# Performance work log

Hardware: AMD Instinct MI355X
Metric: run time of the kernel (lower is better)

## Reference

```python
import jax, jax.numpy as jnp
import numpy as np

BINS = 256
H = 2048
N = 2_000_000


def _tensor2image(x):
    # standard GAN denorm: [-1,1] -> [0,1]
    return (x + 1.0) * 0.5


def _cdf(vals):
    # torch.histc(bins=256, min=0, max=256): unit-width bins, values in [0,255]
    idx = jnp.clip(jnp.floor(vals), 0, BINS - 1).astype(jnp.int32)
    hist = jnp.zeros((BINS,), jnp.float32).at[idx].add(1.0)
    return jnp.cumsum(hist) / hist.sum()


def _trans_table(ref_cdf, adj_cdf):
    # cal_trans: for i in 1..255, first j in 1..255 with adj[j-1] <= ref[i] <= adj[j]
    i_vals = ref_cdf[1:]  # [255]
    cond = (adj_cdf[:-1][None, :] <= i_vals[:, None]) & (i_vals[:, None] <= adj_cdf[1:][None, :])  # [255,255]
    found = cond.any(axis=1)
    first_j = jnp.argmax(cond, axis=1) + 1
    tab = jnp.where(found, first_j, jnp.arange(1, BINS))  # unmatched entries keep identity
    tab = jnp.concatenate([jnp.zeros((1,), tab.dtype), tab])
    tab = tab.at[BINS - 1].set(BINS - 1)
    return tab.astype(jnp.float32)


def _hist_match(dst_img, ref_img, i0, i1, i2, i3):
    # dst_img, ref_img: [3,H,W]; indices: [N]
    dst_align = dst_img[:, i0, i1]  # [3,N]
    ref_align = ref_img[:, i2, i3]  # [3,N]
    cdf_dst = jax.vmap(_cdf)(dst_align)  # [3,256]
    cdf_ref = jax.vmap(_cdf)(ref_align)  # [3,256]
    tables = jax.vmap(_trans_table)(cdf_dst, cdf_ref)  # [3,256]
    bins = jnp.clip(dst_align, 0, BINS - 1).astype(jnp.int32)  # int() truncation on [0,255]
    new_align = jnp.take_along_axis(tables, bins, axis=1)  # [3,N]
    return dst_img.at[:, i0, i1].set(new_align)


def reference(input_data, target_data, mask_src, mask_tar, index0, index1, index2, index3, ref_data):
    inp = _tensor2image(input_data) * 255.0
    tgt = _tensor2image(target_data) * 255.0
    ref = _tensor2image(ref_data) * 255.0
    h = mask_src.shape[2]
    m_src = jnp.broadcast_to(mask_src, (1, 3, h, h))
    m_tar = jnp.broadcast_to(mask_tar, (1, 3, h, h))
    input_masked = inp * m_src
    target_masked = (tgt * m_tar)[0]  # [3,H,W]
    ref_masked = (ref * m_src)[0]     # [3,H,W]
    i0, i1, i2, i3 = index0[0], index1[0], index2[0], index3[0]
    matched = _hist_match(ref_masked, target_masked, i0, i1, i2, i3)[None]  # [1,3,H,W]
    input_match = jax.lax.stop_gradient(matched) * m_src  # no_grad in original
    return jnp.mean((input_masked - input_match) ** 2)


def setup_inputs() -> dict:
    key = jax.random.key(0)
    ks = jax.random.split(key, 9)
    inp = {
        "input_data": jax.random.uniform(ks[0], (1, 3, H, H), jnp.float32, -1.0, 1.0),
        "target_data": jax.random.uniform(ks[1], (1, 3, H, H), jnp.float32, -1.0, 1.0),
        "mask_src": (jax.random.uniform(ks[2], (1, 1, H, H)) > 0.5).astype(jnp.float32),
        "mask_tar": (jax.random.uniform(ks[3], (1, 1, H, H)) > 0.5).astype(jnp.float32),
        "index0": jax.random.randint(ks[4], (1, N), 0, H, jnp.int32),
        "index1": jax.random.randint(ks[5], (1, N), 0, H, jnp.int32),
        "index2": jax.random.randint(ks[6], (1, N), 0, H, jnp.int32),
        "index3": jax.random.randint(ks[7], (1, N), 0, H, jnp.int32),
        "ref_data": jax.random.uniform(ks[8], (1, 3, H, H), jnp.float32, -1.0, 1.0),
    }
    return inp
```

## Files before the change

### kernel.cpp

```cpp
#include <hip/hip_runtime.h>

#define HDIM 2048
#define HH (HDIM * HDIM)
#define NIDX 2000000
#define BINS 256
#define NCOPY 16
#define TL_BLOCKS 2048
#define WH_BLOCKS 2048
#define NWIN 8

#define PART_OFF     0
#define TAB_OFF      16384
#define HIST_OFF     20480
#define PACKED_D_OFF 1048576
#define PACKED_R_OFF 17825792

__global__ __launch_bounds__(256) void pack_kernel(
    const float* __restrict__ ref, const float* __restrict__ tgt,
    const float* __restrict__ msrc, const float* __restrict__ mtar,
    unsigned* __restrict__ packed_d, unsigned* __restrict__ packed_r,
    unsigned* __restrict__ hist)
{
    const int gtid = blockIdx.x * 256 + threadIdx.x;
    const int stride = gridDim.x * 256;

    for (int k = gtid; k < NCOPY * 6 * BINS; k += stride) hist[k] = 0;

    for (int g = gtid; g < HH / 4; g += stride) {
        const int p = g * 4;
        const float4 ms4 = *(const float4*)(msrc + p);
        const float4 mt4 = *(const float4*)(mtar + p);
        const float ms[4] = {ms4.x, ms4.y, ms4.z, ms4.w};
        const float mt[4] = {mt4.x, mt4.y, mt4.z, mt4.w};
        unsigned od[4] = {0, 0, 0, 0}, orr[4] = {0, 0, 0, 0};
#pragma unroll
        for (int c = 0; c < 3; c++) {
            const float4 rv = *(const float4*)(ref + c * HH + p);
            const float4 tv = *(const float4*)(tgt + c * HH + p);
            const float r[4] = {rv.x, rv.y, rv.z, rv.w};
            const float tt[4] = {tv.x, tv.y, tv.z, tv.w};
#pragma unroll
            for (int k = 0; k < 4; k++) {
                const float vd = ((r[k] + 1.0f) * 0.5f) * 255.0f * ms[k];
                const float vr = ((tt[k] + 1.0f) * 0.5f) * 255.0f * mt[k];
                const unsigned bd = (unsigned)(int)fminf(fmaxf(floorf(vd), 0.0f), 255.0f);
                const unsigned br = (unsigned)(int)fminf(fmaxf(floorf(vr), 0.0f), 255.0f);
                od[k]  |= bd << (8 * c);
                orr[k] |= br << (8 * c);
            }
        }
        *(uint4*)(packed_d + p) = make_uint4(od[0], od[1], od[2], od[3]);
        *(uint4*)(packed_r + p) = make_uint4(orr[0], orr[1], orr[2], orr[3]);
    }
}

__global__ __launch_bounds__(256) void whist_kernel(
    unsigned* __restrict__ packed_d, const unsigned* __restrict__ packed_r,
    const int* __restrict__ i0, const int* __restrict__ i1,
    const int* __restrict__ i2, const int* __restrict__ i3,
    unsigned* __restrict__ hist)
{
    __shared__ unsigned lhist[6 * BINS];
    for (int k = threadIdx.x; k < 6 * BINS; k += 256) lhist[k] = 0;
    __syncthreads();

    unsigned z0 = 0, z1 = 0, z2 = 0, z3 = 0, z4 = 0, z5 = 0;
    unsigned char* sampled = (unsigned char*)packed_d;
    const int stride = gridDim.x * 256;

    for (int w = 0; w < NWIN; w++) {
        for (int q = blockIdx.x * 256 + threadIdx.x; q < NIDX / 4; q += stride) {
            const int4 a = ((const int4*)i0)[q];
            const int4 b = ((const int4*)i1)[q];
            const int pd[4] = {a.x * HDIM + b.x, a.y * HDIM + b.y,
                               a.z * HDIM + b.z, a.w * HDIM + b.w};
#pragma unroll
            for (int k = 0; k < 4; k++) {
                if ((pd[k] >> 19) == w) {
                    const unsigned wd = packed_d[pd[k]];
                    sampled[pd[k] * 4 + 3] = 1;
                    const unsigned d0 =  wd        & 255u;
                    const unsigned d1 = (wd >> 8 ) & 255u;
                    const unsigned d2 = (wd >> 16) & 255u;
                    if (d0) atomicAdd(&lhist[           d0], 1u); else z0++;
                    if (d1) atomicAdd(&lhist[1 * BINS + d1], 1u); else z1++;
                    if (d2) atomicAdd(&lhist[2 * BINS + d2], 1u); else z2++;
                }
            }
        }
    }
    for (int w = 0; w < NWIN; w++) {
        for (int q = blockIdx.x * 256 + threadIdx.x; q < NIDX / 4; q += stride) {
            const int4 c = ((const int4*)i2)[q];
            const int4 d = ((const int4*)i3)[q];
            const int pr[4] = {c.x * HDIM + d.x, c.y * HDIM + d.y,
                               c.z * HDIM + d.z, c.w * HDIM + d.w};
#pragma unroll
            for (int k = 0; k < 4; k++) {
                if ((pr[k] >> 19) == w) {
                    const unsigned wr = packed_r[pr[k]];
                    const unsigned r0 =  wr        & 255u;
                    const unsigned r1 = (wr >> 8 ) & 255u;
                    const unsigned r2 = (wr >> 16) & 255u;
                    if (r0) atomicAdd(&lhist[3 * BINS + r0], 1u); else z3++;
                    if (r1) atomicAdd(&lhist[4 * BINS + r1], 1u); else z4++;
                    if (r2) atomicAdd(&lhist[5 * BINS + r2], 1u); else z5++;
                }
            }
        }
    }

    if (z0) atomicAdd(&lhist[0 * BINS], z0);
    if (z1) atomicAdd(&lhist[1 * BINS], z1);
    if (z2) atomicAdd(&lhist[2 * BINS], z2);
    if (z3) atomicAdd(&lhist[3 * BINS], z3);
    if (z4) atomicAdd(&lhist[4 * BINS], z4);
    if (z5) atomicAdd(&lhist[5 * BINS], z5);
    __syncthreads();
    unsigned* h = hist + (blockIdx.x & (NCOPY - 1)) * (6 * BINS);
    for (int k = threadIdx.x; k < 6 * BINS; k += 256) {
        const unsigned v = lhist[k];
        if (v) atomicAdd(&h[k], v);
    }
}

__global__ __launch_bounds__(256) void table_kernel(
    const unsigned* __restrict__ hist, float* __restrict__ tabg)
{
    __shared__ float    cdf[6 * BINS];
    __shared__ unsigned wsum[4];

    const int t    = threadIdx.x;
    const int lane = t & 63;
    const int wid  = t >> 6;

    for (int ch = 0; ch < 6; ch++) {
        unsigned x = 0;
#pragma unroll
        for (int cp = 0; cp < NCOPY; cp++) x += hist[cp * (6 * BINS) + ch * BINS + t];
#pragma unroll
        for (int d = 1; d < 64; d <<= 1) {
            const unsigned y = __shfl_up(x, d, 64);
            if (lane >= d) x += y;
        }
        if (lane == 63) wsum[wid] = x;
        __syncthreads();
        unsigned prefix = 0;
        for (int w = 0; w < wid; w++) prefix += wsum[w];
        x += prefix;
        cdf[ch * BINS + t] = (float)x / 2000000.0f;
        __syncthreads();
    }
    for (int c = 0; c < 3; c++) {
        float o;
        if (t == 0)             o = 0.0f;
        else if (t == BINS - 1) o = 255.0f;
        else {
            const float v = cdf[c * BINS + t];
            const float* arr = cdf + (3 + c) * BINS;
            int lo = 0, hi = 256;
            while (lo < hi) { const int mid = (lo + hi) >> 1; if (arr[mid] < v) lo = mid + 1; else hi = mid; }
            const int J0 = ((lo > 1) ? lo : 1) - 1;
            int lo2 = 0, hi2 = 256;
            while (lo2 < hi2) { const int mid = (lo2 + hi2) >> 1; if (arr[mid] <= v) lo2 = mid + 1; else hi2 = mid; }
            const int J1 = ((lo2 - 1) < 254 ? (lo2 - 1) : 254);
            const bool found = (lo2 >= 1) && (J0 <= J1);
            o = found ? (float)(J0 + 1) : (float)t;
        }
        tabg[c * BINS + t] = o;
    }
}

__global__ __launch_bounds__(256) void tabloss_kernel(
    const float* __restrict__ inp, const float* __restrict__ ref,
    const float* __restrict__ msrc, const float* __restrict__ tabg,
    const unsigned* __restrict__ packed_d, double* __restrict__ partials)
{
    __shared__ float  tab[3 * BINS];
    __shared__ double red[256];

    const int t = threadIdx.x;
    for (int k = t; k < 3 * BINS; k += 256) tab[k] = tabg[k];
    __syncthreads();

    double local = 0.0;
    const int stride = gridDim.x * 256;
    for (int g = blockIdx.x * 256 + t; g < HH / 4; g += stride) {
        const int p = g * 4;
        const float4 mv = *(const float4*)(msrc + p);
        const uint4 pw = *(const uint4*)(packed_d + p);
        const unsigned samp[4] = {pw.x >> 24, pw.y >> 24, pw.z >> 24, pw.w >> 24};
        const float m[4] = {mv.x, mv.y, mv.z, mv.w};
#pragma unroll
        for (int c = 0; c < 3; c++) {
            const float4 rv = *(const float4*)(ref + c * HH + p);
            const float4 iv = *(const float4*)(inp + c * HH + p);
            const float r[4] = {rv.x, rv.y, rv.z, rv.w};
            const float x4[4] = {iv.x, iv.y, iv.z, iv.w};
            float s = 0.0f;
#pragma unroll
            for (int k = 0; k < 4; k++) {
                const float mm = m[k];
                const float refm = ((r[k] + 1.0f) * 0.5f) * 255.0f * mm;
                const float inpm = ((x4[k] + 1.0f) * 0.5f) * 255.0f * mm;
                float matchv;
                if (samp[k]) {
                    const int bidx = (int)fminf(fmaxf(refm, 0.0f), 255.0f);
                    matchv = tab[c * BINS + bidx];
                } else {
                    matchv = refm;
                }
                const float dd = inpm - matchv * mm;
                s += dd * dd;
            }
            local += (double)s;
        }
    }
    red[t] = local;
    __syncthreads();
    for (int s2 = 128; s2 > 0; s2 >>= 1) {
        if (t < s2) red[t] += red[t + s2];
        __syncthreads();
    }
    if (t == 0) partials[blockIdx.x] = red[0];
}

__global__ __launch_bounds__(256) void finalize_kernel(
    const double* __restrict__ partials, float* __restrict__ out)
{
    const int t = threadIdx.x;
    double s = 0.0;
    for (int k = t; k < TL_BLOCKS; k += 256) s += partials[k];
    __shared__ double red[256];
    red[t] = s;
    __syncthreads();
    for (int s2 = 128; s2 > 0; s2 >>= 1) {
        if (t < s2) red[t] += red[t + s2];
        __syncthreads();
    }
    if (t == 0) out[0] = (float)(red[0] / (double)(3 * HH));
}

extern "C" void kernel_launch(void* const* d_in, const int* in_sizes, int n_in,
                              void* d_out, int out_size, void* d_ws, size_t ws_size,
                              hipStream_t stream)
{
    const float* input_data  = (const float*)d_in[0];
    const float* target_data = (const float*)d_in[1];
    const float* mask_src    = (const float*)d_in[2];
    const float* mask_tar    = (const float*)d_in[3];
    const int*   i0          = (const int*)d_in[4];
    const int*   i1          = (const int*)d_in[5];
    const int*   i2          = (const int*)d_in[6];
    const int*   i3          = (const int*)d_in[7];
    const float* ref_data    = (const float*)d_in[8];
    float* out = (float*)d_out;

    char* ws = (char*)d_ws;
    double*   partials = (double*)(ws + PART_OFF);
    float*    tabg     = (float*)(ws + TAB_OFF);
    unsigned* hist     = (unsigned*)(ws + HIST_OFF);
    unsigned* packed_d = (unsigned*)(ws + PACKED_D_OFF);
    unsigned* packed_r = (unsigned*)(ws + PACKED_R_OFF);

    pack_kernel<<<2048, 256, 0, stream>>>(ref_data, target_data, mask_src, mask_tar,
                                          packed_d, packed_r, hist);
    whist_kernel<<<WH_BLOCKS, 256, 0, stream>>>(packed_d, packed_r, i0, i1, i2, i3, hist);
    table_kernel<<<1, 256, 0, stream>>>(hist, tabg);
    tabloss_kernel<<<TL_BLOCKS, 256, 0, stream>>>(input_data, ref_data, mask_src, tabg,
                                                  packed_d, partials);
    finalize_kernel<<<1, 256, 0, stream>>>(partials, out);
}
```

Before: 371.7 us.

## Precompute flat gather indices and move sampled flags to a separate byte array

```diff
diff --git a/kernel.cpp b/kernel.cpp
--- a/kernel.cpp
+++ b/kernel.cpp
@@ -12,19 +12,37 @@
 #define PART_OFF     0
 #define TAB_OFF      16384
 #define HIST_OFF     20480
-#define PACKED_D_OFF 1048576
-#define PACKED_R_OFF 17825792
+#define FLAGS_OFF    131072
+#define PD_OFF       4325376
+#define PR_OFF       12713984
+#define PACKED_D_OFF 21102592
+#define PACKED_R_OFF 37879808
 
 __global__ __launch_bounds__(256) void pack_kernel(
     const float* __restrict__ ref, const float* __restrict__ tgt,
     const float* __restrict__ msrc, const float* __restrict__ mtar,
+    const int* __restrict__ i0, const int* __restrict__ i1,
+    const int* __restrict__ i2, const int* __restrict__ i3,
     unsigned* __restrict__ packed_d, unsigned* __restrict__ packed_r,
-    unsigned* __restrict__ hist)
+    int* __restrict__ pdArr, int* __restrict__ prArr,
+    unsigned* __restrict__ hist, unsigned* __restrict__ flags32)
 {
     const int gtid = blockIdx.x * 256 + threadIdx.x;
     const int stride = gridDim.x * 256;
 
     for (int k = gtid; k < NCOPY * 6 * BINS; k += stride) hist[k] = 0;
+    for (int k = gtid; k < HH / 4; k += stride) flags32[k] = 0;
+
+    for (int s = gtid; s < NIDX / 4; s += stride) {
+        const int4 a = ((const int4*)i0)[s];
+        const int4 b = ((const int4*)i1)[s];
+        const int4 c = ((const int4*)i2)[s];
+        const int4 d = ((const int4*)i3)[s];
+        ((int4*)pdArr)[s] = make_int4(a.x * HDIM + b.x, a.y * HDIM + b.y,
+                                      a.z * HDIM + b.z, a.w * HDIM + b.w);
+        ((int4*)prArr)[s] = make_int4(c.x * HDIM + d.x, c.y * HDIM + d.y,
+                                      c.z * HDIM + d.z, c.w * HDIM + d.w);
+    }
 
     for (int g = gtid; g < HH / 4; g += stride) {
         const int p = g * 4;
@@ -55,30 +73,26 @@
 }
 
 __global__ __launch_bounds__(256) void whist_kernel(
-    unsigned* __restrict__ packed_d, const unsigned* __restrict__ packed_r,
-    const int* __restrict__ i0, const int* __restrict__ i1,
-    const int* __restrict__ i2, const int* __restrict__ i3,
-    unsigned* __restrict__ hist)
+    const unsigned* __restrict__ packed_d, const unsigned* __restrict__ packed_r,
+    const int* __restrict__ pdArr, const int* __restrict__ prArr,
+    unsigned char* __restrict__ flags, unsigned* __restrict__ hist)
 {
     __shared__ unsigned lhist[6 * BINS];
     for (int k = threadIdx.x; k < 6 * BINS; k += 256) lhist[k] = 0;
     __syncthreads();
 
     unsigned z0 = 0, z1 = 0, z2 = 0, z3 = 0, z4 = 0, z5 = 0;
-    unsigned char* sampled = (unsigned char*)packed_d;
     const int stride = gridDim.x * 256;
 
     for (int w = 0; w < NWIN; w++) {
         for (int q = blockIdx.x * 256 + threadIdx.x; q < NIDX / 4; q += stride) {
-            const int4 a = ((const int4*)i0)[q];
-            const int4 b = ((const int4*)i1)[q];
-            const int pd[4] = {a.x * HDIM + b.x, a.y * HDIM + b.y,
-                               a.z * HDIM + b.z, a.w * HDIM + b.w};
+            const int4 pv = ((const int4*)pdArr)[q];
+            const int pd[4] = {pv.x, pv.y, pv.z, pv.w};
 #pragma unroll
             for (int k = 0; k < 4; k++) {
                 if ((pd[k] >> 19) == w) {
                     const unsigned wd = packed_d[pd[k]];
-                    sampled[pd[k] * 4 + 3] = 1;
+                    flags[pd[k]] = 1;
                     const unsigned d0 =  wd        & 255u;
                     const unsigned d1 = (wd >> 8 ) & 255u;
                     const unsigned d2 = (wd >> 16) & 255u;
@@ -91,10 +105,8 @@
     }
     for (int w = 0; w < NWIN; w++) {
         for (int q = blockIdx.x * 256 + threadIdx.x; q < NIDX / 4; q += stride) {
-            const int4 c = ((const int4*)i2)[q];
-            const int4 d = ((const int4*)i3)[q];
-            const int pr[4] = {c.x * HDIM + d.x, c.y * HDIM + d.y,
-                               c.z * HDIM + d.z, c.w * HDIM + d.w};
+            const int4 pv = ((const int4*)prArr)[q];
+            const int pr[4] = {pv.x, pv.y, pv.z, pv.w};
 #pragma unroll
             for (int k = 0; k < 4; k++) {
                 if ((pr[k] >> 19) == w) {
@@ -174,7 +186,7 @@
 __global__ __launch_bounds__(256) void tabloss_kernel(
     const float* __restrict__ inp, const float* __restrict__ ref,
     const float* __restrict__ msrc, const float* __restrict__ tabg,
-    const unsigned* __restrict__ packed_d, double* __restrict__ partials)
+    const unsigned char* __restrict__ flags, double* __restrict__ partials)
 {
     __shared__ float  tab[3 * BINS];
     __shared__ double red[256];
@@ -188,8 +200,8 @@
     for (int g = blockIdx.x * 256 + t; g < HH / 4; g += stride) {
         const int p = g * 4;
         const float4 mv = *(const float4*)(msrc + p);
-        const uint4 pw = *(const uint4*)(packed_d + p);
-        const unsigned samp[4] = {pw.x >> 24, pw.y >> 24, pw.z >> 24, pw.w >> 24};
+        const uchar4 fw = *(const uchar4*)(flags + p);
+        const unsigned samp[4] = {fw.x, fw.y, fw.z, fw.w};
         const float m[4] = {mv.x, mv.y, mv.z, mv.w};
 #pragma unroll
         for (int c = 0; c < 3; c++) {
@@ -257,17 +269,23 @@
     float* out = (float*)d_out;
 
     char* ws = (char*)d_ws;
-    double*   partials = (double*)(ws + PART_OFF);
-    float*    tabg     = (float*)(ws + TAB_OFF);
-    unsigned* hist     = (unsigned*)(ws + HIST_OFF);
-    unsigned* packed_d = (unsigned*)(ws + PACKED_D_OFF);
-    unsigned* packed_r = (unsigned*)(ws + PACKED_R_OFF);
+    double*        partials = (double*)(ws + PART_OFF);
+    float*         tabg     = (float*)(ws + TAB_OFF);
+    unsigned*      hist     = (unsigned*)(ws + HIST_OFF);
+    unsigned*      flags32  = (unsigned*)(ws + FLAGS_OFF);
+    unsigned char* flags    = (unsigned char*)(ws + FLAGS_OFF);
+    int*           pdArr    = (int*)(ws + PD_OFF);
+    int*           prArr    = (int*)(ws + PR_OFF);
+    unsigned*      packed_d = (unsigned*)(ws + PACKED_D_OFF);
+    unsigned*      packed_r = (unsigned*)(ws + PACKED_R_OFF);
 
     pack_kernel<<<2048, 256, 0, stream>>>(ref_data, target_data, mask_src, mask_tar,
-                                          packed_d, packed_r, hist);
-    whist_kernel<<<WH_BLOCKS, 256, 0, stream>>>(packed_d, packed_r, i0, i1, i2, i3, hist);
+                                          i0, i1, i2, i3,
+                                          packed_d, packed_r, pdArr, prArr, hist, flags32);
+    whist_kernel<<<WH_BLOCKS, 256, 0, stream>>>(packed_d, packed_r, pdArr, prArr,
+                                                flags, hist);
     table_kernel<<<1, 256, 0, stream>>>(hist, tabg);
     tabloss_kernel<<<TL_BLOCKS, 256, 0, stream>>>(input_data, ref_data, mask_src, tabg,
-                                                  packed_d, partials);
+                                                  flags, partials);
     finalize_kernel<<<1, 256, 0, stream>>>(partials, out);
 }
```

Result: faster. 334.8 us (-9.9%).

## Bucket-sort gather indices by 64K window before histogram gathers

Applied to the files above, without the earlier changes.

```diff
diff --git a/kernel.cpp b/kernel.cpp
--- a/kernel.cpp
+++ b/kernel.cpp
@@ -6,25 +6,63 @@
 #define BINS 256
 #define NCOPY 16
 #define TL_BLOCKS 2048
-#define WH_BLOCKS 2048
-#define NWIN 8
+#define NCHUNK 2000
+#define CH_I4 250
+#define NWIN 64
 
 #define PART_OFF     0
 #define TAB_OFF      16384
-#define HIST_OFF     20480
-#define PACKED_D_OFF 1048576
-#define PACKED_R_OFF 17825792
+#define WGL_OFF      20480
+#define HIST_OFF     24576
+#define CNT_D_OFF    131072
+#define CNT_R_OFF    393216
+#define OFF_D_OFF    655360
+#define OFF_R_OFF    1179648
+#define FLAGS_OFF    2097152
+#define SORT_D_OFF   6291456
+#define SORT_R_OFF   10485760
+#define PACKED_D_OFF 16777216
+#define PACKED_R_OFF 33554432
 
 __global__ __launch_bounds__(256) void pack_kernel(
     const float* __restrict__ ref, const float* __restrict__ tgt,
     const float* __restrict__ msrc, const float* __restrict__ mtar,
+    const int* __restrict__ i0, const int* __restrict__ i1,
+    const int* __restrict__ i2, const int* __restrict__ i3,
     unsigned* __restrict__ packed_d, unsigned* __restrict__ packed_r,
-    unsigned* __restrict__ hist)
-{
-    const int gtid = blockIdx.x * 256 + threadIdx.x;
+    unsigned* __restrict__ hist, unsigned* __restrict__ flags32,
+    unsigned short* __restrict__ cnt_d, unsigned short* __restrict__ cnt_r)
+{
+    __shared__ unsigned cntd[NWIN], cntr[NWIN];
+    const int t = threadIdx.x;
+    const int gtid = blockIdx.x * 256 + t;
     const int stride = gridDim.x * 256;
 
     for (int k = gtid; k < NCOPY * 6 * BINS; k += stride) hist[k] = 0;
+    for (int k = gtid; k < HH / 4; k += stride) flags32[k] = 0;
+
+    if (blockIdx.x < NCHUNK) {
+        if (t < NWIN) { cntd[t] = 0; cntr[t] = 0; }
+        __syncthreads();
+        if (t < CH_I4) {
+            const int q = blockIdx.x * CH_I4 + t;
+            const int4 a = ((const int4*)i0)[q];
+            const int4 b = ((const int4*)i1)[q];
+            const int4 c = ((const int4*)i2)[q];
+            const int4 d = ((const int4*)i3)[q];
+            const int pd[4] = {a.x * HDIM + b.x, a.y * HDIM + b.y, a.z * HDIM + b.z, a.w * HDIM + b.w};
+            const int pr[4] = {c.x * HDIM + d.x, c.y * HDIM + d.y, c.z * HDIM + d.z, c.w * HDIM + d.w};
+#pragma unroll
+            for (int k = 0; k < 4; k++) atomicAdd(&cntd[pd[k] >> 16], 1u);
+#pragma unroll
+            for (int k = 0; k < 4; k++) atomicAdd(&cntr[pr[k] >> 16], 1u);
+        }
+        __syncthreads();
+        if (t < NWIN) {
+            cnt_d[blockIdx.x * NWIN + t] = (unsigned short)cntd[t];
+            cnt_r[blockIdx.x * NWIN + t] = (unsigned short)cntr[t];
+        }
+    }
 
     for (int g = gtid; g < HH / 4; g += stride) {
         const int p = g * 4;
@@ -54,59 +92,144 @@
     }
 }
 
-__global__ __launch_bounds__(256) void whist_kernel(
-    unsigned* __restrict__ packed_d, const unsigned* __restrict__ packed_r,
+__global__ __launch_bounds__(1024) void off_kernel(
+    const unsigned short* __restrict__ cnt_d, const unsigned short* __restrict__ cnt_r,
+    unsigned* __restrict__ off_d, unsigned* __restrict__ off_r, unsigned* __restrict__ Wg)
+{
+    __shared__ unsigned psum[16][NWIN];
+    __shared__ unsigned segbase[16][NWIN];
+    __shared__ unsigned Wl[NWIN + 1];
+    const int t = threadIdx.x;
+    const int w = t & 63, seg = t >> 6;
+
+    for (int side = 0; side < 2; side++) {
+        const unsigned short* cnt = side ? cnt_r : cnt_d;
+        unsigned* off = side ? off_r : off_d;
+        unsigned s = 0;
+        for (int b = seg * 125; b < seg * 125 + 125; b++) s += cnt[b * NWIN + w];
+        psum[seg][w] = s;
+        __syncthreads();
+        if (t < NWIN) {
+            unsigned run = 0;
+            for (int sg = 0; sg < 16; sg++) { segbase[sg][t] = run; run += psum[sg][t]; }
+            unsigned inc = run;
+            for (int d = 1; d < 64; d <<= 1) {
+                const unsigned y = __shfl_up(inc, d, 64);
+                if (t >= d) inc += y;
+            }
+            Wl[t] = inc - run;
+            if (t == 63) Wl[64] = inc;
+        }
+        __syncthreads();
+        unsigned run = Wl[w] + segbase[seg][w];
+        for (int b = seg * 125; b < seg * 125 + 125; b++) {
+            off[b * NWIN + w] = run;
+            run += cnt[b * NWIN + w];
+        }
+        if (t < NWIN + 1) Wg[side * (NWIN + 1) + t] = Wl[t];
+        __syncthreads();
+    }
+}
+
+__global__ __launch_bounds__(256) void place_kernel(
     const int* __restrict__ i0, const int* __restrict__ i1,
     const int* __restrict__ i2, const int* __restrict__ i3,
-    unsigned* __restrict__ hist)
+    const unsigned* __restrict__ off_d, const unsigned* __restrict__ off_r,
+    unsigned short* __restrict__ sorted_d, unsigned short* __restrict__ sorted_r)
+{
+    __shared__ unsigned cur[NWIN];
+    const int b = blockIdx.x;
+    const int t = threadIdx.x;
+
+    if (t < NWIN) cur[t] = off_d[b * NWIN + t];
+    __syncthreads();
+    if (t < CH_I4) {
+        const int q = b * CH_I4 + t;
+        const int4 a = ((const int4*)i0)[q];
+        const int4 bb = ((const int4*)i1)[q];
+        const int pd[4] = {a.x * HDIM + bb.x, a.y * HDIM + bb.y, a.z * HDIM + bb.z, a.w * HDIM + bb.w};
+#pragma unroll
+        for (int k = 0; k < 4; k++) {
+            const unsigned pos = atomicAdd(&cur[pd[k] >> 16], 1u);
+            sorted_d[pos] = (unsigned short)(pd[k] & 0xFFFF);
+        }
+    }
+    __syncthreads();
+    if (t < NWIN) cur[t] = off_r[b * NWIN + t];
+    __syncthreads();
+    if (t < CH_I4) {
+        const int q = b * CH_I4 + t;
+        const int4 c = ((const int4*)i2)[q];
+        const int4 d = ((const int4*)i3)[q];
+        const int pr[4] = {c.x * HDIM + d.x, c.y * HDIM + d.y, c.z * HDIM + d.z, c.w * HDIM + d.w};
+#pragma unroll
+        for (int k = 0; k < 4; k++) {
+            const unsigned pos = atomicAdd(&cur[pr[k] >> 16], 1u);
+            sorted_r[pos] = (unsigned short)(pr[k] & 0xFFFF);
+        }
+    }
+}
+
+__global__ __launch_bounds__(256) void whist_kernel(
+    const unsigned* __restrict__ packed_d, const unsigned* __restrict__ packed_r,
+    const unsigned short* __restrict__ sorted_d, const unsigned short* __restrict__ sorted_r,
+    const unsigned* __restrict__ Wg,
+    unsigned char* __restrict__ flags, unsigned* __restrict__ hist)
 {
     __shared__ unsigned lhist[6 * BINS];
-    for (int k = threadIdx.x; k < 6 * BINS; k += 256) lhist[k] = 0;
+    __shared__ unsigned Ws[NWIN + 1];
+    const int t = threadIdx.x;
+    for (int k = t; k < 6 * BINS; k += 256) lhist[k] = 0;
+    if (t < NWIN + 1) Ws[t] = Wg[t];
     __syncthreads();
 
     unsigned z0 = 0, z1 = 0, z2 = 0, z3 = 0, z4 = 0, z5 = 0;
-    unsigned char* sampled = (unsigned char*)packed_d;
     const int stride = gridDim.x * 256;
 
-    for (int w = 0; w < NWIN; w++) {
-        for (int q = blockIdx.x * 256 + threadIdx.x; q < NIDX / 4; q += stride) {
-            const int4 a = ((const int4*)i0)[q];
-            const int4 b = ((const int4*)i1)[q];
-            const int pd[4] = {a.x * HDIM + b.x, a.y * HDIM + b.y,
-                               a.z * HDIM + b.z, a.w * HDIM + b.w};
-#pragma unroll
-            for (int k = 0; k < 4; k++) {
-                if ((pd[k] >> 19) == w) {
-                    const unsigned wd = packed_d[pd[k]];
-                    sampled[pd[k] * 4 + 3] = 1;
-                    const unsigned d0 =  wd        & 255u;
-                    const unsigned d1 = (wd >> 8 ) & 255u;
-                    const unsigned d2 = (wd >> 16) & 255u;
-                    if (d0) atomicAdd(&lhist[           d0], 1u); else z0++;
-                    if (d1) atomicAdd(&lhist[1 * BINS + d1], 1u); else z1++;
-                    if (d2) atomicAdd(&lhist[2 * BINS + d2], 1u); else z2++;
-                }
-            }
-        }
-    }
-    for (int w = 0; w < NWIN; w++) {
-        for (int q = blockIdx.x * 256 + threadIdx.x; q < NIDX / 4; q += stride) {
-            const int4 c = ((const int4*)i2)[q];
-            const int4 d = ((const int4*)i3)[q];
-            const int pr[4] = {c.x * HDIM + d.x, c.y * HDIM + d.y,
-                               c.z * HDIM + d.z, c.w * HDIM + d.w};
-#pragma unroll
-            for (int k = 0; k < 4; k++) {
-                if ((pr[k] >> 19) == w) {
-                    const unsigned wr = packed_r[pr[k]];
-                    const unsigned r0 =  wr        & 255u;
-                    const unsigned r1 = (wr >> 8 ) & 255u;
-                    const unsigned r2 = (wr >> 16) & 255u;
-                    if (r0) atomicAdd(&lhist[3 * BINS + r0], 1u); else z3++;
-                    if (r1) atomicAdd(&lhist[4 * BINS + r1], 1u); else z4++;
-                    if (r2) atomicAdd(&lhist[5 * BINS + r2], 1u); else z5++;
-                }
-            }
+    for (int q = blockIdx.x * 256 + t; q < NIDX / 4; q += stride) {
+        const uint2 sv = ((const uint2*)sorted_d)[q];
+        const unsigned lo[4] = {sv.x & 0xFFFFu, sv.x >> 16, sv.y & 0xFFFFu, sv.y >> 16};
+        const unsigned e0 = (unsigned)q * 4u;
+        int wlo = 0, whi = NWIN;
+        while (wlo + 1 < whi) { const int mid = (wlo + whi) >> 1; if (Ws[mid] <= e0) wlo = mid; else whi = mid; }
+        int w = wlo;
+#pragma unroll
+        for (int k = 0; k < 4; k++) {
+            const unsigned e = e0 + k;
+            while (w < NWIN - 1 && Ws[w + 1] <= e) w++;
+            const int pd = (w << 16) | (int)lo[k];
+            const unsigned wd = packed_d[pd];
+            flags[pd] = 1;
+            const unsigned d0 =  wd        & 255u;
+            const unsigned d1 = (wd >> 8 ) & 255u;
+            const unsigned d2 = (wd >> 16) & 255u;
+            if (d0) atomicAdd(&lhist[           d0], 1u); else z0++;
+            if (d1) atomicAdd(&lhist[1 * BINS + d1], 1u); else z1++;
+            if (d2) atomicAdd(&lhist[2 * BINS + d2], 1u); else z2++;
+        }
+    }
+    __syncthreads();
+    if (t < NWIN + 1) Ws[t] = Wg[NWIN + 1 + t];
+    __syncthreads();
+    for (int q = blockIdx.x * 256 + t; q < NIDX / 4; q += stride) {
+        const uint2 sv = ((const uint2*)sorted_r)[q];
+        const unsigned lo[4] = {sv.x & 0xFFFFu, sv.x >> 16, sv.y & 0xFFFFu, sv.y >> 16};
+        const unsigned e0 = (unsigned)q * 4u;
+        int wlo = 0, whi = NWIN;
+        while (wlo + 1 < whi) { const int mid = (wlo + whi) >> 1; if (Ws[mid] <= e0) wlo = mid; else whi = mid; }
+        int w = wlo;
+#pragma unroll
+        for (int k = 0; k < 4; k++) {
+            const unsigned e = e0 + k;
+            while (w < NWIN - 1 && Ws[w + 1] <= e) w++;
+            const int pr = (w << 16) | (int)lo[k];
+            const unsigned wr = packed_r[pr];
+            const unsigned r0 =  wr        & 255u;
+            const unsigned r1 = (wr >> 8 ) & 255u;
+            const unsigned r2 = (wr >> 16) & 255u;
+            if (r0) atomicAdd(&lhist[3 * BINS + r0], 1u); else z3++;
+            if (r1) atomicAdd(&lhist[4 * BINS + r1], 1u); else z4++;
+            if (r2) atomicAdd(&lhist[5 * BINS + r2], 1u); else z5++;
         }
     }
 
@@ -118,7 +241,7 @@
     if (z5) atomicAdd(&lhist[5 * BINS], z5);
     __syncthreads();
     unsigned* h = hist + (blockIdx.x & (NCOPY - 1)) * (6 * BINS);
-    for (int k = threadIdx.x; k < 6 * BINS; k += 256) {
+    for (int k = t; k < 6 * BINS; k += 256) {
         const unsigned v = lhist[k];
         if (v) atomicAdd(&h[k], v);
     }
@@ -174,7 +297,7 @@
 __global__ __launch_bounds__(256) void tabloss_kernel(
     const float* __restrict__ inp, const float* __restrict__ ref,
     const float* __restrict__ msrc, const float* __restrict__ tabg,
-    const unsigned* __restrict__ packed_d, double* __restrict__ partials)
+    const unsigned char* __restrict__ flags, double* __restrict__ partials)
 {
     __shared__ float  tab[3 * BINS];
     __shared__ double red[256];
@@ -188,8 +311,8 @@
     for (int g = blockIdx.x * 256 + t; g < HH / 4; g += stride) {
         const int p = g * 4;
         const float4 mv = *(const float4*)(msrc + p);
-        const uint4 pw = *(const uint4*)(packed_d + p);
-        const unsigned samp[4] = {pw.x >> 24, pw.y >> 24, pw.z >> 24, pw.w >> 24};
+        const uchar4 fw = *(const uchar4*)(flags + p);
+        const unsigned samp[4] = {fw.x, fw.y, fw.z, fw.w};
         const float m[4] = {mv.x, mv.y, mv.z, mv.w};
 #pragma unroll
         for (int c = 0; c < 3; c++) {
@@ -257,17 +380,30 @@
     float* out = (float*)d_out;
 
     char* ws = (char*)d_ws;
-    double*   partials = (double*)(ws + PART_OFF);
-    float*    tabg     = (float*)(ws + TAB_OFF);
-    unsigned* hist     = (unsigned*)(ws + HIST_OFF);
-    unsigned* packed_d = (unsigned*)(ws + PACKED_D_OFF);
-    unsigned* packed_r = (unsigned*)(ws + PACKED_R_OFF);
+    double*         partials = (double*)(ws + PART_OFF);
+    float*          tabg     = (float*)(ws + TAB_OFF);
+    unsigned*       Wg       = (unsigned*)(ws + WGL_OFF);
+    unsigned*       hist     = (unsigned*)(ws + HIST_OFF);
+    unsigned short* cnt_d    = (unsigned short*)(ws + CNT_D_OFF);
+    unsigned short* cnt_r    = (unsigned short*)(ws + CNT_R_OFF);
+    unsigned*       off_d    = (unsigned*)(ws + OFF_D_OFF);
+    unsigned*       off_r    = (unsigned*)(ws + OFF_R_OFF);
+    unsigned*       flags32  = (unsigned*)(ws + FLAGS_OFF);
+    unsigned char*  flags    = (unsigned char*)(ws + FLAGS_OFF);
+    unsigned short* sorted_d = (unsigned short*)(ws + SORT_D_OFF);
+    unsigned short* sorted_r = (unsigned short*)(ws + SORT_R_OFF);
+    unsigned*       packed_d = (unsigned*)(ws + PACKED_D_OFF);
+    unsigned*       packed_r = (unsigned*)(ws + PACKED_R_OFF);
 
     pack_kernel<<<2048, 256, 0, stream>>>(ref_data, target_data, mask_src, mask_tar,
-                                          packed_d, packed_r, hist);
-    whist_kernel<<<WH_BLOCKS, 256, 0, stream>>>(packed_d, packed_r, i0, i1, i2, i3, hist);
+                                          i0, i1, i2, i3,
+                                          packed_d, packed_r, hist, flags32, cnt_d, cnt_r);
+    off_kernel<<<1, 1024, 0, stream>>>(cnt_d, cnt_r, off_d, off_r, Wg);
+    place_kernel<<<NCHUNK, 256, 0, stream>>>(i0, i1, i2, i3, off_d, off_r, sorted_d, sorted_r);
+    whist_kernel<<<2048, 256, 0, stream>>>(packed_d, packed_r, sorted_d, sorted_r, Wg,
+                                           flags, hist);
     table_kernel<<<1, 256, 0, stream>>>(hist, tabg);
     tabloss_kernel<<<TL_BLOCKS, 256, 0, stream>>>(input_data, ref_data, mask_src, tabg,
-                                                  packed_d, partials);
+                                                  flags, partials);
     finalize_kernel<<<1, 256, 0, stream>>>(partials, out);
 }
```

Result: slower. 385.4 us (+3.7%).
